# Optimization experiments

Measured on AMD Instinct MI355X. Metric: run time of the kernel, lower is better.

## Reference

```python
import jax, jax.numpy as jnp
import numpy as np

PATCH_SIZE = 50        # hardcoded in forward (overrides __init__ args)
NUM_PATCHES_OUT = 50   # size of the weighted_x buffer
TOPK = 4


def setup_inputs() -> dict:
    key = jax.random.key(0)
    k1, k2 = jax.random.split(key)
    x = jax.random.normal(k1, (1024, 12, 2500), dtype=jnp.float32)
    # self.weights = sigmoid(sample from N(0,1)) -> a scalar in (0,1)
    weights = jax.nn.sigmoid(jax.random.normal(k2, (), dtype=jnp.float32))
    return {"x": x, "weights": weights}


def reference(x, weights):
    B, N, L = x.shape
    # power spectrum |FFT(x)|^2 along time axis
    power = jnp.abs(jnp.fft.fft(x, axis=2)) ** 2            # [B,N,L] f32
    _, idx = jax.lax.top_k(power, TOPK)                      # [B,N,K] descending
    # only lead 0 and topk positions {0, 2} are used by the original code
    idx2 = idx[:, 0, ::2]                                    # [B,2] int32
    # np.fft.fftfreq(L)[i] = i/L for i <= (L-1)//2 else (i-L)/L
    k_signed = jnp.where(idx2 <= (L - 1) // 2, idx2, idx2 - L)
    valid = k_signed != 0                                    # freq == 0 -> skip
    # ideal_peak_interval = int(|1/freq|) = L // |k| (exact integer math)
    period = L // jnp.maximum(jnp.abs(k_signed), 1)          # [B,2] >= 2
    P = L // PATCH_SIZE                                      # effective num_patches
    starts = jnp.arange(P, dtype=jnp.int32) * PATCH_SIZE     # [P]
    # patch [start, start+PATCH_SIZE) contains a peak (multiple of period)
    # iff the first multiple >= start is < start + PATCH_SIZE
    p = period[..., None]                                    # [B,2,1]
    first_mult = ((starts[None, None, :] + p - 1) // p) * p  # [B,2,P]
    hit = (first_mult < starts[None, None, :] + PATCH_SIZE) & valid[..., None]
    counts = hit.sum(axis=1)                                 # [B,P] in {0,1,2}
    # the b/n loops add `weights` N times per (b, patch, freq-slot) hit
    weighted = (N * weights) * counts.astype(jnp.float32)    # [B,P]
    out = jnp.zeros((B, NUM_PATCHES_OUT), jnp.float32).at[:, :P].set(weighted)
    # original detaches via a numpy round-trip -> no gradient flows
    return jax.lax.stop_gradient(out)
```

## Files before the change

### kernel.cpp

```cpp
#include <hip/hip_runtime.h>

typedef _Float16 f16;
typedef _Float16 f16x2 __attribute__((ext_vector_type(2)));
typedef _Float16 f16x4 __attribute__((ext_vector_type(4)));
typedef _Float16 f16x8 __attribute__((ext_vector_type(8)));
typedef float f32x4 __attribute__((ext_vector_type(4)));

#define L_N 2500
#define B_N 1024
#define ROWSTRIDE 30000
#define NPATCH 50
#define PATCH 50
#define KP 2560
#define NB 2560
#define ZSPLIT 8
#define KS_PER_Z 10

#define TWOPI_F 6.28318530717958647692f
#define RAD_PER_PH (6.283185307179586476925286766559 / 2500.0)

#define OFF_XH 0
#define SZ_XH (B_N * KP * 2)
#define OFF_W  (OFF_XH + SZ_XH)
#define SZ_W   (NB * KP * 2)
#define OFF_C  (OFF_W + SZ_W)
#define SZ_C   (B_N * NB * 4)

#define PB_X    B_N
#define PB_W    1280
#define PB_Z    (SZ_C / 16 / 256)
#define PB_TOT  (PB_X + PB_W + PB_Z)

#define GLOAD16(gp, lp) __builtin_amdgcn_global_load_lds( \
    (const __attribute__((address_space(1))) unsigned int*)(gp), \
    (__attribute__((address_space(3))) unsigned int*)(lp), 16, 0, 0)

__global__ __launch_bounds__(256)
void prep(const float* __restrict__ x, f16* __restrict__ Xh,
          f16* __restrict__ W, float4* __restrict__ C4) {
    const int b = blockIdx.x, tid = threadIdx.x;
    if (b < PB_X) {
        const int row = b;
#pragma unroll
        for (int i = 0; i < 3; ++i) {
            int slot = tid + 256 * i;
            if (slot < 640) {
                float4 v = make_float4(0.f, 0.f, 0.f, 0.f);
                if (slot < 625)
                    v = *reinterpret_cast<const float4*>(x + (size_t)row * ROWSTRIDE + slot * 4);
                f16x4 h = { (f16)v.x, (f16)v.y, (f16)v.z, (f16)v.w };
                *reinterpret_cast<f16x4*>(Xh + (size_t)row * KP + slot * 4) = h;
            }
        }
    } else if (b < PB_X + PB_W) {
        const int bin = b - PB_X;
#pragma unroll
        for (int i = 0; i < 5; ++i) {
            int t2 = tid + 256 * i;
            int t = 2 * t2;
            float c0 = 0.f, s0 = 0.f, c1 = 0.f, s1 = 0.f;
            if (t < L_N) {
                int ph = (bin * t) % L_N;
                float th = (float)ph * (TWOPI_F / (float)L_N);
                __sincosf(th, &s0, &c0);
            }
            if (t + 1 < L_N) {
                int ph = (bin * (t + 1)) % L_N;
                float th = (float)ph * (TWOPI_F / (float)L_N);
                __sincosf(th, &s1, &c1);
            }
            f16x2 cc = { (f16)c0, (f16)c1 };
            f16x2 ss = { (f16)s0, (f16)s1 };
            *reinterpret_cast<f16x2*>(&W[(size_t)(2 * bin) * KP + t])     = cc;
            *reinterpret_cast<f16x2*>(&W[(size_t)(2 * bin + 1) * KP + t]) = ss;
        }
    } else {
        int i = (b - PB_X - PB_W) * 256 + tid;
        C4[i] = make_float4(0.f, 0.f, 0.f, 0.f);
    }
}

__global__ __launch_bounds__(256)
void gemm_f16(const f16* __restrict__ A, const f16* __restrict__ W, float* __restrict__ C) {
    __shared__ f16 As[2][128 * 32];
    __shared__ f16 Bs[2][128 * 32];
    const int tid = threadIdx.x;
    const int wv = tid >> 6, lane = tid & 63;
    const int bm = blockIdx.x, bn = blockIdx.y;
    const int ks0 = blockIdx.z * KS_PER_Z;
    const int wr = wv >> 1, wc = wv & 1;
    const int lrow = lane & 15, lseg = lane >> 4;

    f32x4 acc[4][4];
#pragma unroll
    for (int m = 0; m < 4; ++m)
#pragma unroll
        for (int n = 0; n < 4; ++n) acc[m][n] = (f32x4){0.f, 0.f, 0.f, 0.f};

    const int c0 = wv * 128 + lane, c1 = c0 + 64;
    const int R0 = c0 >> 2, S0 = (c0 & 3) ^ ((R0 >> 1) & 3);
    const int R1 = c1 >> 2, S1 = (c1 & 3) ^ ((R1 >> 1) & 3);
    const f16* ga0 = A + (size_t)(bm * 128 + R0) * KP + S0 * 8;
    const f16* ga1 = A + (size_t)(bm * 128 + R1) * KP + S1 * 8;
    const f16* gb0 = W + (size_t)(bn * 128 + R0) * KP + S0 * 8;
    const f16* gb1 = W + (size_t)(bn * 128 + R1) * KP + S1 * 8;

    int aoff[4], boff[4];
#pragma unroll
    for (int m = 0; m < 4; ++m) {
        int ra = wr * 64 + m * 16 + lrow;
        aoff[m] = ra * 32 + ((lseg ^ ((ra >> 1) & 3)) * 8);
        int rb = wc * 64 + m * 16 + lrow;
        boff[m] = rb * 32 + ((lseg ^ ((rb >> 1) & 3)) * 8);
    }

    {
        const int kof = ks0 * 32;
        GLOAD16(ga0 + kof, &As[0][c0 * 8]);
        GLOAD16(ga1 + kof, &As[0][c1 * 8]);
        GLOAD16(gb0 + kof, &Bs[0][c0 * 8]);
        GLOAD16(gb1 + kof, &Bs[0][c1 * 8]);
    }
    __syncthreads();

    int cur = 0;
    for (int t = 0; t < KS_PER_Z; ++t) {
        const int nxt = cur ^ 1;
        if (t + 1 < KS_PER_Z) {
            const int kof = (ks0 + t + 1) * 32;
            GLOAD16(ga0 + kof, &As[nxt][c0 * 8]);
            GLOAD16(ga1 + kof, &As[nxt][c1 * 8]);
            GLOAD16(gb0 + kof, &Bs[nxt][c0 * 8]);
            GLOAD16(gb1 + kof, &Bs[nxt][c1 * 8]);
        }
        f16x8 af[4], bf[4];
#pragma unroll
        for (int m = 0; m < 4; ++m) af[m] = *(const f16x8*)&As[cur][aoff[m]];
#pragma unroll
        for (int n = 0; n < 4; ++n) bf[n] = *(const f16x8*)&Bs[cur][boff[n]];
#pragma unroll
        for (int m = 0; m < 4; ++m)
#pragma unroll
            for (int n = 0; n < 4; ++n)
                acc[m][n] = __builtin_amdgcn_mfma_f32_16x16x32_f16(af[m], bf[n], acc[m][n], 0, 0, 0);
        __syncthreads();
        cur = nxt;
    }

    const int orow0 = bm * 128 + wr * 64 + (lane >> 4) * 4;
    const int ocol0 = bn * 128 + wc * 64 + (lane & 15);
#pragma unroll
    for (int m = 0; m < 4; ++m)
#pragma unroll
        for (int n = 0; n < 4; ++n)
#pragma unroll
            for (int j = 0; j < 4; ++j)
                atomicAdd(&C[(size_t)(orow0 + m * 16 + j) * NB + ocol0 + n * 16], acc[m][n][j]);
}

__global__ __launch_bounds__(512)
void fused_sel(const float* __restrict__ x, const float* __restrict__ C,
               const float* __restrict__ wp, float* __restrict__ out) {
    __shared__ float xrow[KP];
    __shared__ unsigned long long keybuf[64];
    __shared__ int bins8s[8];
    __shared__ unsigned long long rk[8];
    const int row = blockIdx.x, tid = threadIdx.x;
    const int wv = tid >> 6, lane = tid & 63;

    if (tid < 60) xrow[2500 + tid] = 0.f;
#pragma unroll
    for (int i = 0; i < 2; ++i) {
        int slot = tid + 512 * i;
        if (slot < 625)
            *reinterpret_cast<float4*>(&xrow[slot * 4]) =
                *reinterpret_cast<const float4*>(x + (size_t)row * ROWSTRIDE + slot * 4);
    }

    unsigned long long k3[3];
#pragma unroll
    for (int c = 0; c < 3; ++c) {
        int bin = tid + 512 * c;
        unsigned long long key = 0ULL;
        if (bin <= 1250) {
            float2 ri = *reinterpret_cast<const float2*>(&C[(size_t)row * NB + 2 * bin]);
            float p = ri.x * ri.x + ri.y * ri.y;
            key = ((unsigned long long)__float_as_uint(p) << 32) | (unsigned)(L_N - bin);
        }
        k3[c] = key;
    }
#pragma unroll
    for (int r = 0; r < 8; ++r) {
        unsigned long long m = k3[0];
        m = (k3[1] > m) ? k3[1] : m;
        m = (k3[2] > m) ? k3[2] : m;
#pragma unroll
        for (int off = 32; off > 0; off >>= 1) {
            unsigned long long o = __shfl_xor(m, off, 64);
            m = (o > m) ? o : m;
        }
        if (k3[0] == m) k3[0] = 0ULL;
        if (k3[1] == m) k3[1] = 0ULL;
        if (k3[2] == m) k3[2] = 0ULL;
        if (lane == 0) keybuf[wv * 8 + r] = m;
    }
    __syncthreads();
    if (wv == 0) {
        unsigned long long cur = keybuf[lane];
#pragma unroll
        for (int r = 0; r < 8; ++r) {
            unsigned long long m = cur;
#pragma unroll
            for (int off = 32; off > 0; off >>= 1) {
                unsigned long long o = __shfl_xor(m, off, 64);
                m = (o > m) ? o : m;
            }
            if (cur == m) cur = 0ULL;
            if (lane == 0) bins8s[r] = L_N - (int)(unsigned)(m & 0xffffffffULL);
        }
    }
    __syncthreads();

    const int k = bins8s[wv];
    double c, s, cd, sd;
    {
        int ph0 = (k * lane) % L_N;
        int phd = (k * 64) % L_N;
        sincos((double)ph0 * RAD_PER_PH, &s, &c);
        sincos((double)phd * RAD_PER_PH, &sd, &cd);
    }
    double re = 0.0, im = 0.0;
#pragma unroll 4
    for (int i = 0; i < 40; ++i) {
        double xv = (double)xrow[lane + 64 * i];
        re += xv * c;
        im += xv * s;
        double cn = c * cd - s * sd;
        double sn = s * cd + c * sd;
        c = cn; s = sn;
    }
#pragma unroll
    for (int off = 32; off > 0; off >>= 1) {
        re += __shfl_xor(re, off, 64);
        im += __shfl_xor(im, off, 64);
    }
    if (lane == 0) {
        double p = re * re + im * im;
        unsigned long long pb = (unsigned long long)__double_as_longlong(p);
        rk[wv] = (pb & ~2047ULL) | (unsigned long long)(1250 - k);
    }
    __syncthreads();

    if (tid < NPATCH) {
        unsigned long long q[8];
#pragma unroll
        for (int r = 0; r < 8; ++r) q[r] = rk[r];
        unsigned long long m1 = q[0];
#pragma unroll
        for (int r = 1; r < 8; ++r) m1 = (q[r] > m1) ? q[r] : m1;
#pragma unroll
        for (int r = 0; r < 8; ++r) if (q[r] == m1) q[r] = 0;
        unsigned long long m2 = q[0];
#pragma unroll
        for (int r = 1; r < 8; ++r) m2 = (q[r] > m2) ? q[r] : m2;
#pragma unroll
        for (int r = 0; r < 8; ++r) if (q[r] == m2) q[r] = 0;
        unsigned long long m3 = q[0];
#pragma unroll
        for (int r = 1; r < 8; ++r) m3 = (q[r] > m3) ? q[r] : m3;

        int kA = 1250 - (int)(m1 & 2047ULL);
        int kB = 1250 - (int)(m2 & 2047ULL);
        int kC = 1250 - (int)(m3 & 2047ULL);
        int multA = (kA == 0 || kA == 1250) ? 1 : 2;
        int multB = (kB == 0 || kB == 1250) ? 1 : 2;
        int sel0 = kA;
        int sel1 = (multA == 2 || multB == 2) ? kB : kC;

        int start = tid * PATCH;
        int cnt = 0;
        if (sel0 != 0) {
            int p = L_N / sel0;
            int fm = ((start + p - 1) / p) * p;
            if (fm < start + PATCH) ++cnt;
        }
        if (sel1 != 0) {
            int p = L_N / sel1;
            int fm = ((start + p - 1) / p) * p;
            if (fm < start + PATCH) ++cnt;
        }
        out[(size_t)row * NPATCH + tid] = 12.0f * wp[0] * (float)cnt;
    }
}

extern "C" void kernel_launch(void* const* d_in, const int* in_sizes, int n_in,
                              void* d_out, int out_size, void* d_ws, size_t ws_size,
                              hipStream_t stream) {
    const float* x = (const float*)d_in[0];
    const float* w = (const float*)d_in[1];
    float* out = (float*)d_out;
    char* ws = (char*)d_ws;

    f16* Xh = (f16*)(ws + OFF_XH);
    f16* W  = (f16*)(ws + OFF_W);
    float* C = (float*)(ws + OFF_C);

    prep<<<PB_TOT, 256, 0, stream>>>(x, Xh, W, (float4*)C);
    gemm_f16<<<dim3(8, 20, ZSPLIT), 256, 0, stream>>>(Xh, W, C);
    fused_sel<<<B_N, 512, 0, stream>>>(x, C, w, out);
}
```

Before: 254.5 us.

## Replace split-K atomic accumulation with per-split partial buffers reduced in selection kernel

The GEMM no longer zeros a shared output and atomically adds into it. Each K-split now writes plain stores into its own partial buffer, and the selection kernel sums the partials when it reads real and imaginary parts. The split count also drops from 8 to 4, which gives each block more K work and fewer partials to read back. The cost is a larger workspace, four reads per bin in the selection kernel, and less grid parallelism in the GEMM.

```diff
diff --git a/kernel.cpp b/kernel.cpp
--- a/kernel.cpp
+++ b/kernel.cpp
@@ -13,8 +13,8 @@
 #define PATCH 50
 #define KP 2560
 #define NB 2560
-#define ZSPLIT 8
-#define KS_PER_Z 10
+#define ZSPLIT 4
+#define KS_PER_Z 20
 
 #define TWOPI_F 6.28318530717958647692f
 #define RAD_PER_PH (6.283185307179586476925286766559 / 2500.0)
@@ -23,21 +23,19 @@
 #define SZ_XH (B_N * KP * 2)
 #define OFF_W  (OFF_XH + SZ_XH)
 #define SZ_W   (NB * KP * 2)
-#define OFF_C  (OFF_W + SZ_W)
-#define SZ_C   (B_N * NB * 4)
+#define OFF_P  (OFF_W + SZ_W)
+#define SZ_P   (ZSPLIT * B_N * NB * 4)
 
 #define PB_X    B_N
 #define PB_W    1280
-#define PB_Z    (SZ_C / 16 / 256)
-#define PB_TOT  (PB_X + PB_W + PB_Z)
+#define PB_TOT  (PB_X + PB_W)
 
 #define GLOAD16(gp, lp) __builtin_amdgcn_global_load_lds( \
     (const __attribute__((address_space(1))) unsigned int*)(gp), \
     (__attribute__((address_space(3))) unsigned int*)(lp), 16, 0, 0)
 
 __global__ __launch_bounds__(256)
-void prep(const float* __restrict__ x, f16* __restrict__ Xh,
-          f16* __restrict__ W, float4* __restrict__ C4) {
+void prep(const float* __restrict__ x, f16* __restrict__ Xh, f16* __restrict__ W) {
     const int b = blockIdx.x, tid = threadIdx.x;
     if (b < PB_X) {
         const int row = b;
@@ -52,7 +50,7 @@
                 *reinterpret_cast<f16x4*>(Xh + (size_t)row * KP + slot * 4) = h;
             }
         }
-    } else if (b < PB_X + PB_W) {
+    } else {
         const int bin = b - PB_X;
 #pragma unroll
         for (int i = 0; i < 5; ++i) {
@@ -74,14 +72,11 @@
             *reinterpret_cast<f16x2*>(&W[(size_t)(2 * bin) * KP + t])     = cc;
             *reinterpret_cast<f16x2*>(&W[(size_t)(2 * bin + 1) * KP + t]) = ss;
         }
-    } else {
-        int i = (b - PB_X - PB_W) * 256 + tid;
-        C4[i] = make_float4(0.f, 0.f, 0.f, 0.f);
     }
 }
 
 __global__ __launch_bounds__(256)
-void gemm_f16(const f16* __restrict__ A, const f16* __restrict__ W, float* __restrict__ C) {
+void gemm_f16(const f16* __restrict__ A, const f16* __restrict__ W, float* __restrict__ P) {
     __shared__ f16 As[2][128 * 32];
     __shared__ f16 Bs[2][128 * 32];
     const int tid = threadIdx.x;
@@ -147,6 +142,7 @@
         cur = nxt;
     }
 
+    float* Pz = P + (size_t)blockIdx.z * B_N * NB;
     const int orow0 = bm * 128 + wr * 64 + (lane >> 4) * 4;
     const int ocol0 = bn * 128 + wc * 64 + (lane & 15);
 #pragma unroll
@@ -155,11 +151,11 @@
         for (int n = 0; n < 4; ++n)
 #pragma unroll
             for (int j = 0; j < 4; ++j)
-                atomicAdd(&C[(size_t)(orow0 + m * 16 + j) * NB + ocol0 + n * 16], acc[m][n][j]);
+                Pz[(size_t)(orow0 + m * 16 + j) * NB + ocol0 + n * 16] = acc[m][n][j];
 }
 
 __global__ __launch_bounds__(512)
-void fused_sel(const float* __restrict__ x, const float* __restrict__ C,
+void fused_sel(const float* __restrict__ x, const float* __restrict__ P,
                const float* __restrict__ wp, float* __restrict__ out) {
     __shared__ float xrow[KP];
     __shared__ unsigned long long keybuf[64];
@@ -183,8 +179,14 @@
         int bin = tid + 512 * c;
         unsigned long long key = 0ULL;
         if (bin <= 1250) {
-            float2 ri = *reinterpret_cast<const float2*>(&C[(size_t)row * NB + 2 * bin]);
-            float p = ri.x * ri.x + ri.y * ri.y;
+            float re = 0.f, im = 0.f;
+#pragma unroll
+            for (int s2 = 0; s2 < ZSPLIT; ++s2) {
+                float2 ri = *reinterpret_cast<const float2*>(
+                    &P[((size_t)s2 * B_N + row) * NB + 2 * bin]);
+                re += ri.x; im += ri.y;
+            }
+            float p = re * re + im * im;
             key = ((unsigned long long)__float_as_uint(p) << 32) | (unsigned)(L_N - bin);
         }
         k3[c] = key;
@@ -303,9 +305,9 @@
 
     f16* Xh = (f16*)(ws + OFF_XH);
     f16* W  = (f16*)(ws + OFF_W);
-    float* C = (float*)(ws + OFF_C);
-
-    prep<<<PB_TOT, 256, 0, stream>>>(x, Xh, W, (float4*)C);
-    gemm_f16<<<dim3(8, 20, ZSPLIT), 256, 0, stream>>>(Xh, W, C);
-    fused_sel<<<B_N, 512, 0, stream>>>(x, C, w, out);
+    float* P = (float*)(ws + OFF_P);
+
+    prep<<<PB_TOT, 256, 0, stream>>>(x, Xh, W);
+    gemm_f16<<<dim3(8, 20, ZSPLIT), 256, 0, stream>>>(Xh, W, P);
+    fused_sel<<<B_N, 512, 0, stream>>>(x, P, w, out);
 }
```

After: 208.1 us. 18.2% less time.
